# Kernel tuning notes

Measured on AMD Instinct MI355X. Metric: run time of the kernel, lower is better.

The kernel has to match this reference:

```python
import jax, jax.numpy as jnp
import numpy as np

B, T, D, F, E, K = 2, 1024, 1024, 2048, 8, 2

def setup_inputs() -> dict:
    key = jax.random.key(0)
    ks = jax.random.split(key, 9)
    s = 0.02
    return {
        "states": jax.random.normal(ks[0], (B, T, D), dtype=jnp.float32),
        "Wg": jax.random.normal(ks[1], (D, E), dtype=jnp.float32) * s,
        "W_in": jax.random.normal(ks[2], (E, D, F), dtype=jnp.float32) * s,
        "b_in": jnp.zeros((E, F), dtype=jnp.float32),
        "W_scale": jax.random.normal(ks[3], (E, D, F), dtype=jnp.float32) * s,
        "b_scale": jnp.zeros((E, F), dtype=jnp.float32),
        "W_out": jax.random.normal(ks[4], (E, F, D), dtype=jnp.float32) * s,
        "b_out": jnp.zeros((E, D), dtype=jnp.float32),
        "num_selected": K,
    }

def reference(states, Wg, W_in, b_in, W_scale, b_scale, W_out, b_out, num_selected):
    b, t, d = states.shape
    x = states.reshape(-1, d)                      # [N, D]
    n = x.shape[0]
    # router: softmax over experts, then top-k + renormalize
    probs = jax.nn.softmax(x @ Wg, axis=-1)        # [N, E]
    topw, topi = jax.lax.top_k(probs, num_selected)  # [N, K]
    topw = topw / topw.sum(axis=-1, keepdims=True)
    # dense combine weights [N, E]: zero except selected experts
    w_full = jnp.zeros_like(probs).at[jnp.arange(n)[:, None], topi].set(topw)
    # gated-GELU expert MLPs, batched over experts
    h = jnp.einsum('nd,edf->enf', x, W_in) + b_in[:, None, :]       # [E, N, F]
    s = jnp.einsum('nd,edf->enf', x, W_scale) + b_scale[:, None, :]
    inner = jax.nn.gelu(h, approximate=False) * s                    # exact GELU (torch default)
    y = jnp.einsum('enf,efd->end', inner, W_out) + b_out[:, None, :]  # [E, N, D]
    out = jnp.einsum('end,ne->nd', y, w_full)                         # weighted combine
    return out.reshape(b, t, d)
```

## Files before the change

kernel.cpp:

```cpp
#include <hip/hip_runtime.h>
#include <hip/hip_bf16.h>
#include <math.h>

#define N_TOK 2048
#define DIM   1024
#define FF    2048
#define NEXP  8
#define NSLOT (N_TOK * 2)
#define NCVT  3072

typedef __attribute__((ext_vector_type(8))) short short8;
typedef __attribute__((ext_vector_type(4))) float f32x4;
typedef _Float16 half_t;
typedef __attribute__((ext_vector_type(4))) _Float16 h16x4;

__device__ __forceinline__ unsigned short f2bf(float f) {
    unsigned int u = __float_as_uint(f);
    u += 0x7FFFu + ((u >> 16) & 1u);
    return (unsigned short)(u >> 16);
}

#define GLOAD_LDS16(g, l) \
    __builtin_amdgcn_global_load_lds((const __attribute__((address_space(1))) unsigned int*)(g), \
                                     (__attribute__((address_space(3))) unsigned int*)(l), 16, 0, 0)

__global__ __launch_bounds__(256) void k_prep(
        const float* __restrict__ x, const float* __restrict__ Wg,
        const float* __restrict__ Win, const float* __restrict__ Wsc,
        const float* __restrict__ Wout,
        unsigned short* __restrict__ wt_h, unsigned short* __restrict__ wt_s,
        unsigned short* __restrict__ wt_o,
        int* __restrict__ hdr, int* __restrict__ tok_e,
        float* __restrict__ tok_w, int* __restrict__ tok_slot,
        unsigned short* __restrict__ xg, int mode) {
    __shared__ unsigned short sh[64][260];
    int gid = blockIdx.x;
    int t = threadIdx.x;

    if (gid < NCVT) {
        int bz = gid >> 7;
        int which = bz >> 3, e = bz & 7;
        int R = (which == 2) ? FF : DIM;
        int C = (which == 2) ? DIM : FF;
        const float* S = ((which == 0) ? Win : (which == 1) ? Wsc : Wout)
                         + (size_t)e * DIM * FF;
        unsigned short* D = ((which == 0) ? wt_h : (which == 1) ? wt_s : wt_o)
                            + (size_t)e * DIM * FF;
        int local = gid & 127;
        int tilesx = C >> 6;
        int tx = local % tilesx, ty = local / tilesx;
        int c0 = tx * 64, r0 = ty * 256;
        int rl = t >> 4, cl = (t & 15) * 4;
#pragma unroll
        for (int p = 0; p < 16; ++p) {
            int r = p * 16 + rl;
            float4 v = *(const float4*)(S + (size_t)(r0 + r) * C + c0 + cl);
            sh[cl + 0][r] = f2bf(v.x);
            sh[cl + 1][r] = f2bf(v.y);
            sh[cl + 2][r] = f2bf(v.z);
            sh[cl + 3][r] = f2bf(v.w);
        }
        __syncthreads();
        int ol = t >> 5, wl = (t & 31) * 8;
#pragma unroll
        for (int q = 0; q < 8; ++q) {
            int oc = q * 8 + ol;
            uint2 lo = *(const uint2*)&sh[oc][wl];
            uint2 hi = *(const uint2*)&sh[oc][wl + 4];
            *(uint4*)(D + (size_t)(c0 + oc) * R + r0 + wl) =
                make_uint4(lo.x, lo.y, hi.x, hi.y);
        }
        return;
    }

    int rblk = gid - NCVT;
    int wave = t >> 6, lane = t & 63;
    int tok = rblk * 4 + wave;
    if (mode && gid == NCVT && t < NEXP) hdr[16 + t] = t * N_TOK;

    float acc[NEXP];
#pragma unroll
    for (int e = 0; e < NEXP; ++e) acc[e] = 0.f;
    const float* xr = x + (size_t)tok * DIM;
    for (int d = lane; d < DIM; d += 64) {
        float xv = xr[d];
        const float* wr = Wg + d * NEXP;
#pragma unroll
        for (int e = 0; e < NEXP; ++e) acc[e] += xv * wr[e];
    }
#pragma unroll
    for (int off = 32; off > 0; off >>= 1) {
#pragma unroll
        for (int e = 0; e < NEXP; ++e) acc[e] += __shfl_down(acc[e], off);
    }
    int s0 = 0, s1 = 0;
    if (lane == 0) {
        int e0 = 0;
#pragma unroll
        for (int e = 1; e < NEXP; ++e) if (acc[e] > acc[e0]) e0 = e;
        int e1 = -1;
#pragma unroll
        for (int e = 0; e < NEXP; ++e) {
            if (e == e0) continue;
            if (e1 < 0 || acc[e] > acc[e1]) e1 = e;
        }
        float w0 = 1.f / (1.f + expf(acc[e1] - acc[e0]));
        tok_e[2 * tok] = e0; tok_e[2 * tok + 1] = e1;
        tok_w[2 * tok] = w0; tok_w[2 * tok + 1] = 1.f - w0;
        if (mode) {
            int p0 = atomicAdd(&hdr[e0], 1);
            int p1 = atomicAdd(&hdr[e1], 1);
            s0 = e0 * N_TOK + p0; s1 = e1 * N_TOK + p1;
            tok_slot[2 * tok] = s0; tok_slot[2 * tok + 1] = s1;
        } else {
            atomicAdd(&hdr[e0], 1);
            atomicAdd(&hdr[e1], 1);
        }
    }
    if (mode) {
        s0 = __shfl(s0, 0); s1 = __shfl(s1, 0);
        const float4* xv4 = (const float4*)xr;
#pragma unroll
        for (int j = 0; j < 4; ++j) {
            float4 v = xv4[lane + j * 64];
            ushort4 b;
            b.x = f2bf(v.x); b.y = f2bf(v.y); b.z = f2bf(v.z); b.w = f2bf(v.w);
            ((ushort4*)(xg + (size_t)s0 * DIM))[lane + j * 64] = b;
            ((ushort4*)(xg + (size_t)s1 * DIM))[lane + j * 64] = b;
        }
    }
}

__global__ void k_scan(int* hdr) {
    if (threadIdx.x == 0 && blockIdx.x == 0) {
        int s = 0;
        for (int e = 0; e < NEXP; ++e) {
            hdr[16 + e] = s;
            hdr[8 + e]  = s;
            s += hdr[e];
        }
        hdr[24] = s;
    }
}

__global__ __launch_bounds__(256) void k_assign(const float* __restrict__ x,
        int* __restrict__ hdr, const int* __restrict__ tok_e,
        int* __restrict__ tok_slot, unsigned short* __restrict__ xg) {
    __shared__ int sh[2];
    int t = blockIdx.x;
    if (threadIdx.x == 0) {
        int e0 = tok_e[2 * t], e1 = tok_e[2 * t + 1];
        int p0 = atomicAdd(&hdr[8 + e0], 1);
        int p1 = atomicAdd(&hdr[8 + e1], 1);
        tok_slot[2 * t] = p0; tok_slot[2 * t + 1] = p1;
        sh[0] = p0; sh[1] = p1;
    }
    __syncthreads();
    int s0 = sh[0], s1 = sh[1];
    const float4* xr = (const float4*)(x + (size_t)t * DIM);
    float4 v = xr[threadIdx.x];
    ushort4 b;
    b.x = f2bf(v.x); b.y = f2bf(v.y); b.z = f2bf(v.z); b.w = f2bf(v.w);
    ((ushort4*)(xg + (size_t)s0 * DIM))[threadIdx.x] = b;
    ((ushort4*)(xg + (size_t)s1 * DIM))[threadIdx.x] = b;
}

__global__ __launch_bounds__(256, 4) void k_expert_hs(
        const unsigned short* __restrict__ xg,
        const unsigned short* __restrict__ Wth,
        const unsigned short* __restrict__ Wts,
        const float* __restrict__ b_in, const float* __restrict__ b_sc,
        const int* __restrict__ hdr, unsigned short* __restrict__ inner) {
    int e = blockIdx.z;
    int cnt = hdr[e];
    int mtile = blockIdx.y;
    if (mtile * 128 >= cnt) return;
    int base = hdr[16 + e];
    int f0 = blockIdx.x * 64;

    __shared__ unsigned short As[2 * 128 * 32];
    __shared__ unsigned short Bh[2 * 64 * 32];
    __shared__ unsigned short Bs[2 * 64 * 32];

    int tid = threadIdx.x;
    int wave = tid >> 6, lane = tid & 63;
    int lr = lane & 15, lq = lane >> 4;
    int wm = (wave >> 1) * 64, wf = (wave & 1) * 32;

    f32x4 acch[4][2], accs[4][2];
#pragma unroll
    for (int mi = 0; mi < 4; ++mi)
#pragma unroll
        for (int fi = 0; fi < 2; ++fi) {
            acch[mi][fi] = (f32x4){0.f, 0.f, 0.f, 0.f};
            accs[mi][fi] = (f32x4){0.f, 0.f, 0.f, 0.f};
        }

    int swzc = (lane & 3) ^ ((lane >> 3) & 3);
    int goff = (lane >> 2) * DIM + swzc * 8;
    int rdo = lr * 32 + (lq ^ ((lr >> 1) & 3)) * 8;

    const unsigned short* Abase = xg  + (size_t)(base + mtile * 128) * DIM + goff;
    const unsigned short* Hbase = Wth + ((size_t)e * FF + f0) * DIM + goff;
    const unsigned short* Sbase = Wts + ((size_t)e * FF + f0) * DIM + goff;
    int pa0 = wave * 16, pa1 = 64 + wave * 16, pb = wave * 16;

    GLOAD_LDS16(Abase + (size_t)pa0 * DIM, &As[pa0 * 32]);
    GLOAD_LDS16(Abase + (size_t)pa1 * DIM, &As[pa1 * 32]);
    GLOAD_LDS16(Hbase + (size_t)pb * DIM, &Bh[pb * 32]);
    GLOAD_LDS16(Sbase + (size_t)pb * DIM, &Bs[pb * 32]);
    __syncthreads();

    const int NSTEP = DIM / 32;
    for (int t = 0; t < NSTEP; ++t) {
        int coA = (t & 1) * (128 * 32), coB = (t & 1) * (64 * 32);
        if (t + 1 < NSTEP) {
            int noA = ((t & 1) ^ 1) * (128 * 32), noB = ((t & 1) ^ 1) * (64 * 32);
            int k1 = (t + 1) * 32;
            GLOAD_LDS16(Abase + (size_t)pa0 * DIM + k1, &As[noA + pa0 * 32]);
            GLOAD_LDS16(Abase + (size_t)pa1 * DIM + k1, &As[noA + pa1 * 32]);
            GLOAD_LDS16(Hbase + (size_t)pb * DIM + k1, &Bh[noB + pb * 32]);
            GLOAD_LDS16(Sbase + (size_t)pb * DIM + k1, &Bs[noB + pb * 32]);
        }

        short8 af[4], bhf[2], bsf[2];
#pragma unroll
        for (int mi = 0; mi < 4; ++mi)
            af[mi] = *(const short8*)&As[coA + (wm + mi * 16) * 32 + rdo];
#pragma unroll
        for (int fi = 0; fi < 2; ++fi) {
            bhf[fi] = *(const short8*)&Bh[coB + (wf + fi * 16) * 32 + rdo];
            bsf[fi] = *(const short8*)&Bs[coB + (wf + fi * 16) * 32 + rdo];
        }
#pragma unroll
        for (int mi = 0; mi < 4; ++mi)
#pragma unroll
            for (int fi = 0; fi < 2; ++fi) {
                acch[mi][fi] = __builtin_amdgcn_mfma_f32_16x16x32_bf16(
                    af[mi], bhf[fi], acch[mi][fi], 0, 0, 0);
                accs[mi][fi] = __builtin_amdgcn_mfma_f32_16x16x32_bf16(
                    af[mi], bsf[fi], accs[mi][fi], 0, 0, 0);
            }
        __syncthreads();
    }

#pragma unroll
    for (int fi = 0; fi < 2; ++fi) {
        int f = f0 + wf + fi * 16 + lr;
        float bi = b_in[e * FF + f];
        float bs2 = b_sc[e * FF + f];
#pragma unroll
        for (int mi = 0; mi < 4; ++mi) {
#pragma unroll
            for (int r = 0; r < 4; ++r) {
                int rl = wm + mi * 16 + lq * 4 + r;
                int grow = mtile * 128 + rl;
                if (grow < cnt) {
                    float h = acch[mi][fi][r] + bi;
                    float s = accs[mi][fi][r] + bs2;
                    float g = 0.5f * h * (1.f + erff(h * 0.70710678f));
                    inner[(size_t)(base + grow) * FF + f] = f2bf(g * s);
                }
            }
        }
    }
}

__global__ __launch_bounds__(256, 4) void k_expert_out(
        const unsigned short* __restrict__ inner,
        const unsigned short* __restrict__ Wto,
        const int* __restrict__ hdr, half_t* __restrict__ pbuf, int pstride) {
    int e = blockIdx.z & 7;
    int ks = blockIdx.z >> 3;
    int cnt = hdr[e];
    int mtile = blockIdx.y;
    if (mtile * 128 >= cnt) return;
    int base = hdr[16 + e];
    int d0 = blockIdx.x * 128;

    __shared__ unsigned short As[2 * 128 * 32];
    __shared__ unsigned short Bt[2 * 128 * 32];

    int tid = threadIdx.x;
    int wave = tid >> 6, lane = tid & 63;
    int lr = lane & 15, lq = lane >> 4;
    int wm = (wave >> 1) * 64, wn = (wave & 1) * 64;

    f32x4 acc[4][4];
#pragma unroll
    for (int mi = 0; mi < 4; ++mi)
#pragma unroll
        for (int ni = 0; ni < 4; ++ni) acc[mi][ni] = (f32x4){0.f, 0.f, 0.f, 0.f};

    int swzc = (lane & 3) ^ ((lane >> 3) & 3);
    int goff = (lane >> 2) * FF + swzc * 8;
    int rdo = lr * 32 + (lq ^ ((lr >> 1) & 3)) * 8;

    const unsigned short* Abase = inner + (size_t)(base + mtile * 128) * FF + goff;
    const unsigned short* Bbase = Wto + ((size_t)e * DIM + d0) * FF + goff;
    int pa0 = wave * 16, pa1 = 64 + wave * 16;

    int kbeg = ks * (FF / 2);

    GLOAD_LDS16(Abase + (size_t)pa0 * FF + kbeg, &As[pa0 * 32]);
    GLOAD_LDS16(Abase + (size_t)pa1 * FF + kbeg, &As[pa1 * 32]);
    GLOAD_LDS16(Bbase + (size_t)pa0 * FF + kbeg, &Bt[pa0 * 32]);
    GLOAD_LDS16(Bbase + (size_t)pa1 * FF + kbeg, &Bt[pa1 * 32]);
    __syncthreads();

    const int NSTEP = (FF / 2) / 32;
    for (int t = 0; t < NSTEP; ++t) {
        int co = (t & 1) * (128 * 32);
        if (t + 1 < NSTEP) {
            int no = ((t & 1) ^ 1) * (128 * 32);
            int k1 = kbeg + (t + 1) * 32;
            GLOAD_LDS16(Abase + (size_t)pa0 * FF + k1, &As[no + pa0 * 32]);
            GLOAD_LDS16(Abase + (size_t)pa1 * FF + k1, &As[no + pa1 * 32]);
            GLOAD_LDS16(Bbase + (size_t)pa0 * FF + k1, &Bt[no + pa0 * 32]);
            GLOAD_LDS16(Bbase + (size_t)pa1 * FF + k1, &Bt[no + pa1 * 32]);
        }

        short8 af[4], bfm[4];
#pragma unroll
        for (int mi = 0; mi < 4; ++mi)
            af[mi] = *(const short8*)&As[co + (wm + mi * 16) * 32 + rdo];
#pragma unroll
        for (int ni = 0; ni < 4; ++ni)
            bfm[ni] = *(const short8*)&Bt[co + (wn + ni * 16) * 32 + rdo];
#pragma unroll
        for (int mi = 0; mi < 4; ++mi)
#pragma unroll
            for (int ni = 0; ni < 4; ++ni)
                acc[mi][ni] = __builtin_amdgcn_mfma_f32_16x16x32_bf16(
                    af[mi], bfm[ni], acc[mi][ni], 0, 0, 0);
        __syncthreads();
    }

    half_t* P = pbuf + (size_t)ks * pstride * DIM;
#pragma unroll
    for (int ni = 0; ni < 4; ++ni) {
        int d = d0 + wn + ni * 16 + lr;
#pragma unroll
        for (int mi = 0; mi < 4; ++mi) {
#pragma unroll
            for (int r = 0; r < 4; ++r) {
                int rl = wm + mi * 16 + lq * 4 + r;
                int grow = mtile * 128 + rl;
                if (grow < cnt)
                    P[(size_t)(base + grow) * DIM + d] = (half_t)acc[mi][ni][r];
            }
        }
    }
}

__global__ __launch_bounds__(256) void k_combine(const half_t* __restrict__ pbuf,
        const int* __restrict__ tok_slot, const int* __restrict__ tok_e,
        const float* __restrict__ tok_w, const float* __restrict__ b_out,
        float* __restrict__ out, int pstride) {
    int t = blockIdx.x;
    int d = threadIdx.x * 4;
    int s0 = tok_slot[2 * t], s1 = tok_slot[2 * t + 1];
    int e0 = tok_e[2 * t], e1 = tok_e[2 * t + 1];
    float w0 = tok_w[2 * t], w1 = tok_w[2 * t + 1];
    const half_t* pA = pbuf;
    const half_t* pB = pbuf + (size_t)pstride * DIM;
    h16x4 a0 = *(const h16x4*)&pA[(size_t)s0 * DIM + d];
    h16x4 a1 = *(const h16x4*)&pB[(size_t)s0 * DIM + d];
    h16x4 c0 = *(const h16x4*)&pA[(size_t)s1 * DIM + d];
    h16x4 c1 = *(const h16x4*)&pB[(size_t)s1 * DIM + d];
    float4 b0 = *(const float4*)&b_out[e0 * DIM + d];
    float4 b1 = *(const float4*)&b_out[e1 * DIM + d];
    float4 r;
    r.x = w0 * ((float)a0.x + (float)a1.x + b0.x) + w1 * ((float)c0.x + (float)c1.x + b1.x);
    r.y = w0 * ((float)a0.y + (float)a1.y + b0.y) + w1 * ((float)c0.y + (float)c1.y + b1.y);
    r.z = w0 * ((float)a0.z + (float)a1.z + b0.z) + w1 * ((float)c0.z + (float)c1.z + b1.z);
    r.w = w0 * ((float)a0.w + (float)a1.w + b0.w) + w1 * ((float)c0.w + (float)c1.w + b1.w);
    *(float4*)&out[(size_t)t * DIM + d] = r;
}

extern "C" void kernel_launch(void* const* d_in, const int* in_sizes, int n_in,
                              void* d_out, int out_size, void* d_ws, size_t ws_size,
                              hipStream_t stream) {
    (void)in_sizes; (void)n_in; (void)out_size;
    const float* x    = (const float*)d_in[0];
    const float* Wg   = (const float*)d_in[1];
    const float* Win  = (const float*)d_in[2];
    const float* b_in = (const float*)d_in[3];
    const float* Wsc  = (const float*)d_in[4];
    const float* b_sc = (const float*)d_in[5];
    const float* Wout = (const float*)d_in[6];
    const float* b_out= (const float*)d_in[7];
    float* out = (float*)d_out;

    char* ws = (char*)d_ws;
    int*   hdr      = (int*)ws;
    int*   tok_e    = (int*)(ws + 256);
    float* tok_w    = (float*)(ws + 16640);
    int*   tok_slot = (int*)(ws + 33024);

    const size_t BIG_NEED = 65792ULL + (32ULL + 64 + 64 + 96) * 1024 * 1024;
    int big = (ws_size >= BIG_NEED) ? 1 : 0;

    unsigned short *xg, *inner, *wt_h, *wt_s, *wt_o;
    half_t* pbuf;
    int slab;
    if (big) {
        xg    = (unsigned short*)(ws + 65792);
        inner = (unsigned short*)(ws + 65792 + 33554432);
        pbuf  = (half_t*)(ws + 65792 + 33554432 + 67108864);
        wt_h  = (unsigned short*)(ws + 65792 + 33554432 + 67108864 + 67108864);
        wt_s  = wt_h + (size_t)NEXP * FF * DIM;
        wt_o  = wt_s + (size_t)NEXP * FF * DIM;
        slab  = NEXP * N_TOK;
    } else {
        xg    = (unsigned short*)(ws + 65792);
        inner = (unsigned short*)(ws + 65792 + 8388608);
        pbuf  = (half_t*)(ws + 65792 + 8388608 + 16777216);
        wt_h  = (unsigned short*)(ws + 65792 + 8388608 + 16777216 + 16777216);
        wt_s  = wt_h + (size_t)NEXP * FF * DIM;
        wt_o  = wt_s + (size_t)NEXP * FF * DIM;
        slab  = NSLOT;
    }

    hipMemsetAsync(hdr, 0, 256, stream);
    k_prep<<<dim3(NCVT + N_TOK / 4), dim3(256), 0, stream>>>(
        x, Wg, Win, Wsc, Wout, wt_h, wt_s, wt_o,
        hdr, tok_e, tok_w, tok_slot, xg, big);
    if (!big) {
        k_scan<<<dim3(1), dim3(64), 0, stream>>>(hdr);
        k_assign<<<dim3(N_TOK), dim3(256), 0, stream>>>(x, hdr, tok_e, tok_slot, xg);
    }
    k_expert_hs<<<dim3(FF / 64, 16, NEXP), dim3(256), 0, stream>>>(
        xg, wt_h, wt_s, b_in, b_sc, hdr, inner);
    k_expert_out<<<dim3(DIM / 128, 16, NEXP * 2), dim3(256), 0, stream>>>(
        inner, wt_o, hdr, pbuf, slab);
    k_combine<<<dim3(N_TOK), dim3(256), 0, stream>>>(
        pbuf, tok_slot, tok_e, tok_w, b_out, out, slab);
}
```

Baseline: 437.3 us.

## Pre-tile and pre-swizzle expert weights into LDS-ready contiguous blocks

The prep kernel now writes the bf16 expert weights as contiguous 64x32 (or 128x32) tiles in the exact swizzled order the GEMM's LDS layout expects, using four times as many smaller conversion blocks. The two GEMM kernels then load each B tile with fully contiguous per-wave 16-byte global-to-LDS transfers instead of strided row loads. This is meant to improve coalescing and cut address arithmetic on the weight stream. The cost is more prep blocks and a layout coupling that must stay consistent with the GEMM tile shapes.

Result: faster. 428.3 us (-2.1%).

```diff
diff --git a/kernel.cpp b/kernel.cpp
--- a/kernel.cpp
+++ b/kernel.cpp
@@ -7,7 +7,7 @@
 #define FF    2048
 #define NEXP  8
 #define NSLOT (N_TOK * 2)
-#define NCVT  3072
+#define NCVT  12288
 
 typedef __attribute__((ext_vector_type(8))) short short8;
 typedef __attribute__((ext_vector_type(4))) float f32x4;
@@ -33,42 +33,61 @@
         int* __restrict__ hdr, int* __restrict__ tok_e,
         float* __restrict__ tok_w, int* __restrict__ tok_slot,
         unsigned short* __restrict__ xg, int mode) {
-    __shared__ unsigned short sh[64][260];
+    __shared__ unsigned short sh[64][72];
     int gid = blockIdx.x;
     int t = threadIdx.x;
 
     if (gid < NCVT) {
-        int bz = gid >> 7;
-        int which = bz >> 3, e = bz & 7;
-        int R = (which == 2) ? FF : DIM;
-        int C = (which == 2) ? DIM : FF;
-        const float* S = ((which == 0) ? Win : (which == 1) ? Wsc : Wout)
-                         + (size_t)e * DIM * FF;
-        unsigned short* D = ((which == 0) ? wt_h : (which == 1) ? wt_s : wt_o)
-                            + (size_t)e * DIM * FF;
-        int local = gid & 127;
-        int tilesx = C >> 6;
-        int tx = local % tilesx, ty = local / tilesx;
-        int c0 = tx * 64, r0 = ty * 256;
+        int which = gid >> 12;
+        int local = gid & 4095;
+        int e = local >> 9;
+        int rem = local & 511;
         int rl = t >> 4, cl = (t & 15) * 4;
-#pragma unroll
-        for (int p = 0; p < 16; ++p) {
-            int r = p * 16 + rl;
-            float4 v = *(const float4*)(S + (size_t)(r0 + r) * C + c0 + cl);
-            sh[cl + 0][r] = f2bf(v.x);
-            sh[cl + 1][r] = f2bf(v.y);
-            sh[cl + 2][r] = f2bf(v.z);
-            sh[cl + 3][r] = f2bf(v.w);
-        }
-        __syncthreads();
-        int ol = t >> 5, wl = (t & 31) * 8;
-#pragma unroll
-        for (int q = 0; q < 8; ++q) {
-            int oc = q * 8 + ol;
-            uint2 lo = *(const uint2*)&sh[oc][wl];
-            uint2 hi = *(const uint2*)&sh[oc][wl + 4];
-            *(uint4*)(D + (size_t)(c0 + oc) * R + r0 + wl) =
-                make_uint4(lo.x, lo.y, hi.x, hi.y);
+        if (which < 2) {
+            int ft = rem >> 4, kg = rem & 15;
+            const float* S = ((which == 0) ? Win : Wsc) + (size_t)e * DIM * FF
+                             + (size_t)(kg * 64) * FF + ft * 64;
+            unsigned short* D = ((which == 0) ? wt_h : wt_s)
+                                + (((size_t)e * 32 + ft) * 32 + kg * 2) * 2048;
+#pragma unroll
+            for (int p = 0; p < 4; ++p) {
+                int k = p * 16 + rl;
+                float4 v = *(const float4*)(S + (size_t)k * FF + cl);
+                sh[cl + 0][k] = f2bf(v.x);
+                sh[cl + 1][k] = f2bf(v.y);
+                sh[cl + 2][k] = f2bf(v.z);
+                sh[cl + 3][k] = f2bf(v.w);
+            }
+            __syncthreads();
+            int r = t >> 2, c = t & 3;
+#pragma unroll
+            for (int p2 = 0; p2 < 2; ++p2) {
+                int ks = p2 * 32 + ((c ^ ((r >> 1) & 3)) * 8);
+                *(uint4*)(D + (size_t)p2 * 2048 + t * 8) = *(const uint4*)&sh[r][ks];
+            }
+        } else {
+            int dg = rem >> 5, kg = rem & 31;
+            const float* S = Wout + (size_t)e * DIM * FF
+                             + (size_t)(kg * 64) * DIM + dg * 64;
+            int dt = dg >> 1, o = (dg & 1) * 64;
+            unsigned short* D = wt_o + (((size_t)e * 8 + dt) * 64 + kg * 2) * 4096
+                                + o * 32;
+#pragma unroll
+            for (int p = 0; p < 4; ++p) {
+                int k = p * 16 + rl;
+                float4 v = *(const float4*)(S + (size_t)k * DIM + cl);
+                sh[cl + 0][k] = f2bf(v.x);
+                sh[cl + 1][k] = f2bf(v.y);
+                sh[cl + 2][k] = f2bf(v.z);
+                sh[cl + 3][k] = f2bf(v.w);
+            }
+            __syncthreads();
+            int r = t >> 2, c = t & 3;
+#pragma unroll
+            for (int p2 = 0; p2 < 2; ++p2) {
+                int ks = p2 * 32 + ((c ^ ((r >> 1) & 3)) * 8);
+                *(uint4*)(D + (size_t)p2 * 4096 + t * 8) = *(const uint4*)&sh[r][ks];
+            }
         }
         return;
     }
@@ -76,7 +95,7 @@
     int rblk = gid - NCVT;
     int wave = t >> 6, lane = t & 63;
     int tok = rblk * 4 + wave;
-    if (mode && gid == NCVT && t < NEXP) hdr[16 + t] = t * N_TOK;
+    if (mode && rblk == 0 && t < NEXP) hdr[16 + t] = t * N_TOK;
 
     float acc[NEXP];
 #pragma unroll
@@ -201,14 +220,17 @@
     int rdo = lr * 32 + (lq ^ ((lr >> 1) & 3)) * 8;
 
     const unsigned short* Abase = xg  + (size_t)(base + mtile * 128) * DIM + goff;
-    const unsigned short* Hbase = Wth + ((size_t)e * FF + f0) * DIM + goff;
-    const unsigned short* Sbase = Wts + ((size_t)e * FF + f0) * DIM + goff;
-    int pa0 = wave * 16, pa1 = 64 + wave * 16, pb = wave * 16;
+    const unsigned short* Hp = Wth + (((size_t)e * 32 + (f0 >> 6)) * 32) * 2048
+                               + wave * 512 + lane * 8;
+    const unsigned short* Sp = Wts + (((size_t)e * 32 + (f0 >> 6)) * 32) * 2048
+                               + wave * 512 + lane * 8;
+    int pa0 = wave * 16, pa1 = 64 + wave * 16;
+    int wb = wave * 512;
 
     GLOAD_LDS16(Abase + (size_t)pa0 * DIM, &As[pa0 * 32]);
     GLOAD_LDS16(Abase + (size_t)pa1 * DIM, &As[pa1 * 32]);
-    GLOAD_LDS16(Hbase + (size_t)pb * DIM, &Bh[pb * 32]);
-    GLOAD_LDS16(Sbase + (size_t)pb * DIM, &Bs[pb * 32]);
+    GLOAD_LDS16(Hp, &Bh[wb]);
+    GLOAD_LDS16(Sp, &Bs[wb]);
     __syncthreads();
 
     const int NSTEP = DIM / 32;
@@ -219,8 +241,8 @@
             int k1 = (t + 1) * 32;
             GLOAD_LDS16(Abase + (size_t)pa0 * DIM + k1, &As[noA + pa0 * 32]);
             GLOAD_LDS16(Abase + (size_t)pa1 * DIM + k1, &As[noA + pa1 * 32]);
-            GLOAD_LDS16(Hbase + (size_t)pb * DIM + k1, &Bh[noB + pb * 32]);
-            GLOAD_LDS16(Sbase + (size_t)pb * DIM + k1, &Bs[noB + pb * 32]);
+            GLOAD_LDS16(Hp + (size_t)(t + 1) * 2048, &Bh[noB + wb]);
+            GLOAD_LDS16(Sp + (size_t)(t + 1) * 2048, &Bs[noB + wb]);
         }
 
         short8 af[4], bhf[2], bsf[2];
@@ -297,15 +319,17 @@
     int rdo = lr * 32 + (lq ^ ((lr >> 1) & 3)) * 8;
 
     const unsigned short* Abase = inner + (size_t)(base + mtile * 128) * FF + goff;
-    const unsigned short* Bbase = Wto + ((size_t)e * DIM + d0) * FF + goff;
+    const unsigned short* Bp = Wto + ((((size_t)e * 8 + (d0 >> 7)) * 64 + (size_t)ks * 32)) * 4096
+                               + wave * 512 + lane * 8;
     int pa0 = wave * 16, pa1 = 64 + wave * 16;
+    int wb = wave * 512;
 
     int kbeg = ks * (FF / 2);
 
     GLOAD_LDS16(Abase + (size_t)pa0 * FF + kbeg, &As[pa0 * 32]);
     GLOAD_LDS16(Abase + (size_t)pa1 * FF + kbeg, &As[pa1 * 32]);
-    GLOAD_LDS16(Bbase + (size_t)pa0 * FF + kbeg, &Bt[pa0 * 32]);
-    GLOAD_LDS16(Bbase + (size_t)pa1 * FF + kbeg, &Bt[pa1 * 32]);
+    GLOAD_LDS16(Bp, &Bt[wb]);
+    GLOAD_LDS16(Bp + 2048, &Bt[2048 + wb]);
     __syncthreads();
 
     const int NSTEP = (FF / 2) / 32;
@@ -316,8 +340,8 @@
             int k1 = kbeg + (t + 1) * 32;
             GLOAD_LDS16(Abase + (size_t)pa0 * FF + k1, &As[no + pa0 * 32]);
             GLOAD_LDS16(Abase + (size_t)pa1 * FF + k1, &As[no + pa1 * 32]);
-            GLOAD_LDS16(Bbase + (size_t)pa0 * FF + k1, &Bt[no + pa0 * 32]);
-            GLOAD_LDS16(Bbase + (size_t)pa1 * FF + k1, &Bt[no + pa1 * 32]);
+            GLOAD_LDS16(Bp + (size_t)(t + 1) * 4096, &Bt[no + wb]);
+            GLOAD_LDS16(Bp + (size_t)(t + 1) * 4096 + 2048, &Bt[no + 2048 + wb]);
         }
 
         short8 af[4], bfm[4];
```
